# Optimization experiments

Measured on AMD Instinct MI355X. Metric: run time of the kernel, lower is better.

Reference implementation:

```python
import jax, jax.numpy as jnp
import numpy as np

B, T, N, DIN, HID, EMB, K, HOR, ODIM = 64, 12, 883, 1, 64, 10, 2, 12, 1


def setup_inputs() -> dict:
    key = jax.random.key(0)
    ks = jax.random.split(key, 12)
    s = 0.1  # keep gate pre-activations sane
    return dict(
        source=jax.random.normal(ks[0], (B, T, N, DIN), jnp.float32),
        node_emb=jax.random.normal(ks[1], (N, EMB), jnp.float32),
        w0_g=jax.random.normal(ks[2], (EMB, K, DIN + HID, 2 * HID), jnp.float32) * s,
        b0_g=jax.random.normal(ks[3], (EMB, 2 * HID), jnp.float32) * s,
        w0_c=jax.random.normal(ks[4], (EMB, K, DIN + HID, HID), jnp.float32) * s,
        b0_c=jax.random.normal(ks[5], (EMB, HID), jnp.float32) * s,
        w1_g=jax.random.normal(ks[6], (EMB, K, 2 * HID, 2 * HID), jnp.float32) * s,
        b1_g=jax.random.normal(ks[7], (EMB, 2 * HID), jnp.float32) * s,
        w1_c=jax.random.normal(ks[8], (EMB, K, 2 * HID, HID), jnp.float32) * s,
        b1_c=jax.random.normal(ks[9], (EMB, HID), jnp.float32) * s,
        conv_w=jax.random.normal(ks[10], (HOR * ODIM, 1, 1, HID), jnp.float32) * s,
        conv_b=jax.random.normal(ks[11], (HOR * ODIM,), jnp.float32) * s,
    )


def _supports(E):
    # adaptive adjacency: softmax(relu(E E^T)) row-wise, Chebyshev set [I, A, ...]
    A = jax.nn.softmax(jax.nn.relu(E @ E.T), axis=1)
    sup = [jnp.eye(E.shape[0], dtype=A.dtype), A]
    for _ in range(2, K):
        sup.append(2.0 * (A @ sup[-1]) - sup[-2])
    return jnp.stack(sup)  # [K, N, N]


def _gconv(x, E, sup, wpool, bpool):
    # x: [B,N,Cin] -> [B,N,Cout]; node-specific weights pooled from embeddings
    w = jnp.einsum('nd,dkio->nkio', E, wpool)          # [N,K,Cin,Cout]
    b = E @ bpool                                      # [N,Cout]
    xg = jnp.einsum('knm,bmc->bnkc', sup, x)           # [B,N,K,Cin]
    return jnp.einsum('bnki,nkio->bno', xg, w) + b


def _cell(x, h, E, sup, wg, bg, wc, bc):
    zr = jax.nn.sigmoid(_gconv(jnp.concatenate([x, h], -1), E, sup, wg, bg))
    z, r = jnp.split(zr, 2, axis=-1)
    hc = jnp.tanh(_gconv(jnp.concatenate([x, z * h], -1), E, sup, wc, bc))
    return r * h + (1.0 - r) * hc


def reference(source, node_emb, w0_g, b0_g, w0_c, b0_c, w1_g, b1_g, w1_c, b1_c, conv_w, conv_b):
    sup = _supports(node_emb)
    cur = jnp.transpose(source, (1, 0, 2, 3))  # [T,B,N,C]
    for wg, bg, wc, bc in ((w0_g, b0_g, w0_c, b0_c), (w1_g, b1_g, w1_c, b1_c)):
        h0 = jnp.zeros((source.shape[0], N, HID), source.dtype)

        def step(h, xt, wg=wg, bg=bg, wc=wc, bc=bc):
            hn = _cell(xt, h, node_emb, sup, wg, bg, wc, bc)
            return hn, hn

        _, cur = jax.lax.scan(step, h0, cur)  # [T,B,N,HID]
    last = cur[-1]  # [B,N,HID]
    # Conv2d(1, HOR*ODIM, kernel=(1,HID)) over [B,1,N,HID] == contraction over HID
    out = jnp.einsum('bnh,oh->bon', last, conv_w[:, 0, 0, :]) + conv_b[None, :, None]
    out = out.reshape(-1, HOR, ODIM, N).transpose(0, 1, 3, 2)  # [B,HOR,N,ODIM]
    return out
```

## Files before the change

kernel.cpp:

```cpp
#include <hip/hip_runtime.h>
#include <cstddef>

#define NN 883
#define BB 64
#define TT 12
#define EMB 10
#define KPAD 896

typedef short short8 __attribute__((ext_vector_type(8)));
typedef _Float16 half8 __attribute__((ext_vector_type(8)));
typedef float f32x4 __attribute__((ext_vector_type(4)));

__device__ __forceinline__ void split_f16(float v, _Float16* hp, _Float16* lp) {
  _Float16 h = (_Float16)v;
  *hp = h;
  *lp = (_Float16)(v - (float)h);
}

__global__ __launch_bounds__(256) void adj_kernel(const float* __restrict__ E,
                                                  _Float16* __restrict__ Ah,
                                                  _Float16* __restrict__ Al) {
  const int n = blockIdx.x;
  const int tid = threadIdx.x;
  __shared__ float sE[EMB];
  __shared__ float sred[256];
  if (tid < EMB) sE[tid] = E[n * EMB + tid];
  __syncthreads();
  float d[4];
  float lmax = 0.0f;
#pragma unroll
  for (int q = 0; q < 4; ++q) {
    int m = tid + q * 256;
    d[q] = 0.0f;
    if (m < NN) {
      float s = 0.0f;
#pragma unroll
      for (int e = 0; e < EMB; ++e) s += sE[e] * E[m * EMB + e];
      d[q] = fmaxf(s, 0.0f);
      lmax = fmaxf(lmax, d[q]);
    }
  }
  sred[tid] = lmax;
  __syncthreads();
  for (int s = 128; s > 0; s >>= 1) {
    if (tid < s) sred[tid] = fmaxf(sred[tid], sred[tid + s]);
    __syncthreads();
  }
  const float mx = sred[0];
  __syncthreads();
  float lsum = 0.0f;
#pragma unroll
  for (int q = 0; q < 4; ++q) {
    int m = tid + q * 256;
    if (m < NN) {
      d[q] = expf(d[q] - mx);
      lsum += d[q];
    }
  }
  sred[tid] = lsum;
  __syncthreads();
  for (int s = 128; s > 0; s >>= 1) {
    if (tid < s) sred[tid] += sred[tid + s];
    __syncthreads();
  }
  const float inv = 1.0f / sred[0];
#pragma unroll
  for (int q = 0; q < 4; ++q) {
    int m = tid + q * 256;
    if (m < KPAD) {
      float v = (m < NN) ? d[q] * inv : 0.0f;
      split_f16(v, &Ah[(size_t)n * KPAD + m], &Al[(size_t)n * KPAD + m]);
    }
  }
}

__global__ __launch_bounds__(256) void mfma_gemm3(const _Float16* __restrict__ Ah,
                                                  const _Float16* __restrict__ Al,
                                                  const _Float16* __restrict__ Xh,
                                                  const _Float16* __restrict__ Xl,
                                                  _Float16* __restrict__ Gh,
                                                  _Float16* __restrict__ Gl, int L) {
  __shared__ _Float16 sA[2][128][40];
  __shared__ _Float16 sX[2][4][128][8];
  const int tid = threadIdx.x;
  const int lane = tid & 63;
  const int wid = tid >> 6;
  const int wm = (wid >> 1) * 64, wn = (wid & 1) * 64;
  const int bm = blockIdx.y * 128;
  const int bl = blockIdx.x * 128;
  const int l15 = lane & 15, l4 = lane >> 4;

  f32x4 acc[4][4] = {};

  const int xlp = (tid & 63) * 2;
  const int xko = tid >> 6;

  for (int k0 = 0; k0 < KPAD; k0 += 32) {
    __syncthreads();
#pragma unroll
    for (int p = 0; p < 2; ++p) {
      int i = tid + p * 256;
      int m = i >> 2, k8 = (i & 3) * 8;
      *(half8*)&sA[0][m][k8] = *(const half8*)&Ah[(size_t)(bm + m) * KPAD + k0 + k8];
      *(half8*)&sA[1][m][k8] = *(const half8*)&Al[(size_t)(bm + m) * KPAD + k0 + k8];
    }
    {
      int gl = bl + xlp;
      int kb = k0 + xko * 8;
#pragma unroll
      for (int buf = 0; buf < 2; ++buf) {
        const _Float16* Xp = buf ? Xl : Xh;
        unsigned int v[8];
#pragma unroll
        for (int j = 0; j < 8; ++j)
          v[j] = *(const unsigned int*)&Xp[(size_t)(kb + j) * L + gl];
        short8 lo, hi;
#pragma unroll
        for (int j = 0; j < 8; ++j) {
          lo[j] = (short)(v[j] & 0xFFFFu);
          hi[j] = (short)(v[j] >> 16);
        }
        *(short8*)&sX[buf][xko][xlp][0] = lo;
        *(short8*)&sX[buf][xko][xlp + 1][0] = hi;
      }
    }
    __syncthreads();
    half8 afh[4], afl[4], bfh[4], bfl[4];
#pragma unroll
    for (int mi = 0; mi < 4; ++mi) {
      afh[mi] = *(half8*)&sA[0][wm + mi * 16 + l15][l4 * 8];
      afl[mi] = *(half8*)&sA[1][wm + mi * 16 + l15][l4 * 8];
    }
#pragma unroll
    for (int ni = 0; ni < 4; ++ni) {
      bfh[ni] = *(half8*)&sX[0][l4][wn + ni * 16 + l15][0];
      bfl[ni] = *(half8*)&sX[1][l4][wn + ni * 16 + l15][0];
    }
#pragma unroll
    for (int mi = 0; mi < 4; ++mi)
#pragma unroll
      for (int ni = 0; ni < 4; ++ni) {
        acc[mi][ni] = __builtin_amdgcn_mfma_f32_16x16x32_f16(afh[mi], bfh[ni],
                                                             acc[mi][ni], 0, 0, 0);
        acc[mi][ni] = __builtin_amdgcn_mfma_f32_16x16x32_f16(afh[mi], bfl[ni],
                                                             acc[mi][ni], 0, 0, 0);
        acc[mi][ni] = __builtin_amdgcn_mfma_f32_16x16x32_f16(afl[mi], bfh[ni],
                                                             acc[mi][ni], 0, 0, 0);
      }
  }
#pragma unroll
  for (int mi = 0; mi < 4; ++mi) {
    int row0 = bm + wm + mi * 16 + l4 * 4;
#pragma unroll
    for (int ni = 0; ni < 4; ++ni) {
      int col = bl + wn + ni * 16 + l15;
#pragma unroll
      for (int r = 0; r < 4; ++r) {
        int row = row0 + r;
        if (row < NN)
          split_f16(acc[mi][ni][r], &Gh[(size_t)row * L + col],
                    &Gl[(size_t)row * L + col]);
      }
    }
  }
}

__global__ __launch_bounds__(256) void srcall_kernel(const float* __restrict__ src,
                                                     _Float16* __restrict__ Xsh,
                                                     _Float16* __restrict__ Xsl) {
  int i = blockIdx.x * 256 + threadIdx.x;
  if (i >= NN * BB * TT) return;
  int t = i % TT;
  int nb = i / TT;
  int b = nb & 63, n = nb >> 6;
  float v = src[((size_t)b * TT + t) * NN + n];
  size_t idx = (size_t)n * (TT * 512) + (size_t)t * 512 + (size_t)b * 8;
  split_f16(v, &Xsh[idx], &Xsl[idx]);
}

template <int CS, int CIN, int XSPLIT, int OW, int COUT>
__global__ __launch_bounds__(256) void wgen_pre(const float* __restrict__ E,
                                                const float* __restrict__ wpool,
                                                _Float16* __restrict__ Wh,
                                                _Float16* __restrict__ Wl) {
  constexpr int C = COUT / OW;
  constexpr int KD = 2 * CS;
  constexpr int KOW = KD / 8;
  const int bid = blockIdx.x;
  const int n = bid / C;
  const int oc = bid % C;
  if (n >= NN) return;
  const int och = oc * OW;
  const int tid = threadIdx.x;
  __shared__ float sE[EMB];
  if (tid < EMB) sE[tid] = E[n * EMB + tid];
  __syncthreads();
  _Float16* bh = Wh + ((size_t)n * C + oc) * ((size_t)KOW * OW * 8);
  _Float16* bl = Wl + ((size_t)n * C + oc) * ((size_t)KOW * OW * 8);
  const int o = tid & (OW - 1);
  for (int ko = tid / OW; ko < KOW; ko += 256 / OW) {
    half8 hv, lv;
#pragma unroll
    for (int j = 0; j < 8; ++j) {
      const int k = ko * 8 + j;
      const int kk = (k >= CS) ? 1 : 0;
      const int kc = k - kk * CS;
      int ii;
      if (CS == CIN) ii = kc;
      else ii = (kc == 0) ? 0 : ((kc >= XSPLIT) ? kc - XSPLIT + 1 : -1);
      float w = 0.0f;
      if (ii >= 0) {
        const float* wp = wpool + ((size_t)kk * CIN + ii) * COUT + och + o;
#pragma unroll
        for (int d = 0; d < EMB; ++d)
          w += sE[d] * wp[(size_t)d * (2 * CIN * COUT)];
      }
      _Float16 hh = (_Float16)w;
      hv[j] = hh;
      lv[j] = (_Float16)(w - (float)hh);
    }
    *(half8*)&bh[((size_t)ko * OW + o) * 8] = hv;
    *(half8*)&bl[((size_t)ko * OW + o) * 8] = lv;
  }
}

template <int CS, int CIN, int XSPLIT, int OW, bool GATE>
__global__ __launch_bounds__(256) void gconv_fused(
    const _Float16* __restrict__ IXh, const _Float16* __restrict__ IXl, int sIX, int oIX,
    const _Float16* __restrict__ IZh, const _Float16* __restrict__ IZl, int sIZ, int oIZ,
    const _Float16* __restrict__ DXh, const _Float16* __restrict__ DXl, int sDX, int oDX,
    const _Float16* __restrict__ DZh, const _Float16* __restrict__ DZl, int sDZ, int oDZ,
    const float* __restrict__ E, const float* __restrict__ wpool,
    const float* __restrict__ bpool, const float* __restrict__ ZRin,
    float* __restrict__ hstate, float* __restrict__ ZRout,
    _Float16* __restrict__ XAh, _Float16* __restrict__ XAl, int csA, int cbA,
    const _Float16* __restrict__ PWh, const _Float16* __restrict__ PWl) {
  constexpr int COUT = GATE ? 128 : 64;
  constexpr int C = COUT / OW;
  constexpr int KD = 2 * CS;
  constexpr int KP = (KD + 31) & ~31;
  constexpr int KOW = KD / 8;
  constexpr int NT = OW / 32;
  const int bid = blockIdx.x;
  const int xcd = bid & 7;
  const int rest = bid >> 3;
  const int oc = rest % C;
  const int nq = rest / C;
  const int n = nq * 8 + xcd;
  if (n >= NN) return;
  const int och = oc * OW;
  const int tid = threadIdx.x;
  const int lane = tid & 63, wid = tid >> 6;
  const int wm = (wid & 1) * 32;
  const int wn = (wid >> 1) * (OW / 2);
  const int l15 = lane & 15, l4 = lane >> 4;

  __shared__ float sE[EMB];
  __shared__ float sB[OW];
  __shared__ _Float16 sWh[KOW * OW * 8];
  __shared__ _Float16 sWl[KOW * OW * 8];

  if (tid < EMB) sE[tid] = E[n * EMB + tid];
  __syncthreads();

  if (PWh != nullptr) {
    const size_t wbase = ((size_t)n * C + oc) * ((size_t)KOW * OW * 8);
    for (int i = tid; i < KOW * OW; i += 256) {
      *(half8*)&sWh[(size_t)i * 8] = *(const half8*)&PWh[wbase + (size_t)i * 8];
      *(half8*)&sWl[(size_t)i * 8] = *(const half8*)&PWl[wbase + (size_t)i * 8];
    }
  } else {
    const int o = tid & (OW - 1);
    for (int ko = tid / OW; ko < KOW; ko += 256 / OW) {
      half8 hv, lv;
#pragma unroll
      for (int j = 0; j < 8; ++j) {
        const int k = ko * 8 + j;
        const int kk = (k >= CS) ? 1 : 0;
        const int kc = k - kk * CS;
        int ii;
        if (CS == CIN) ii = kc;
        else ii = (kc == 0) ? 0 : ((kc >= XSPLIT) ? kc - XSPLIT + 1 : -1);
        float w = 0.0f;
        if (ii >= 0) {
          const float* wp = wpool + ((size_t)kk * CIN + ii) * COUT + och + o;
#pragma unroll
          for (int d = 0; d < EMB; ++d)
            w += sE[d] * wp[(size_t)d * (2 * CIN * COUT)];
        }
        _Float16 hh = (_Float16)w;
        hv[j] = hh;
        lv[j] = (_Float16)(w - (float)hh);
      }
      *(half8*)&sWh[((size_t)ko * OW + o) * 8] = hv;
      *(half8*)&sWl[((size_t)ko * OW + o) * 8] = lv;
    }
  }
  if (tid < OW) {
    float bb = 0.0f;
#pragma unroll
    for (int d = 0; d < EMB; ++d) bb += sE[d] * bpool[d * COUT + och + tid];
    sB[tid] = bb;
  }
  __syncthreads();

  const size_t bIX = (size_t)n * sIX + (size_t)oIX * 512;
  const size_t bIZ = (size_t)n * sIZ + (size_t)oIZ * 512;
  const size_t bDX = (size_t)n * sDX + (size_t)oDX * 512;
  const size_t bDZ = (size_t)n * sDZ + (size_t)oDZ * 512;
  f32x4 acc[2][NT] = {};
  for (int k0 = 0; k0 < KP; k0 += 32) {
    const int kq = k0 + l4 * 8;
    half8 ah[2], al[2];
#pragma unroll
    for (int mt = 0; mt < 2; ++mt) {
      const int b = wm + mt * 16 + l15;
      if (kq < XSPLIT) {
        const size_t o = bIX + (size_t)(kq >> 3) * 512 + (size_t)b * 8;
        ah[mt] = *(const half8*)&IXh[o];
        al[mt] = *(const half8*)&IXl[o];
      } else if (kq < CS) {
        const size_t o = bIZ + (size_t)((kq - XSPLIT) >> 3) * 512 + (size_t)b * 8;
        ah[mt] = *(const half8*)&IZh[o];
        al[mt] = *(const half8*)&IZl[o];
      } else if (kq < CS + XSPLIT) {
        const size_t o = bDX + (size_t)((kq - CS) >> 3) * 512 + (size_t)b * 8;
        ah[mt] = *(const half8*)&DXh[o];
        al[mt] = *(const half8*)&DXl[o];
      } else if (kq < KD) {
        const size_t o =
            bDZ + (size_t)((kq - CS - XSPLIT) >> 3) * 512 + (size_t)b * 8;
        ah[mt] = *(const half8*)&DZh[o];
        al[mt] = *(const half8*)&DZl[o];
      } else {
        ah[mt] = (half8)(_Float16)0.f;
        al[mt] = (half8)(_Float16)0.f;
      }
    }
    const int koi = kq >> 3;
#pragma unroll
    for (int nt = 0; nt < NT; ++nt) {
      const int ol = wn + nt * 16 + l15;
      half8 bh, bl;
      if constexpr (KP == KD) {
        bh = *(const half8*)&sWh[((size_t)koi * OW + ol) * 8];
        bl = *(const half8*)&sWl[((size_t)koi * OW + ol) * 8];
      } else {
        if (kq < KD) {
          bh = *(const half8*)&sWh[((size_t)koi * OW + ol) * 8];
          bl = *(const half8*)&sWl[((size_t)koi * OW + ol) * 8];
        } else {
          bh = (half8)(_Float16)0.f;
          bl = (half8)(_Float16)0.f;
        }
      }
#pragma unroll
      for (int mt = 0; mt < 2; ++mt) {
        acc[mt][nt] =
            __builtin_amdgcn_mfma_f32_16x16x32_f16(ah[mt], bh, acc[mt][nt], 0, 0, 0);
        acc[mt][nt] =
            __builtin_amdgcn_mfma_f32_16x16x32_f16(ah[mt], bl, acc[mt][nt], 0, 0, 0);
        acc[mt][nt] =
            __builtin_amdgcn_mfma_f32_16x16x32_f16(al[mt], bh, acc[mt][nt], 0, 0, 0);
      }
    }
  }

#pragma unroll
  for (int mt = 0; mt < 2; ++mt) {
#pragma unroll
    for (int nt = 0; nt < NT; ++nt) {
      const int ol = wn + nt * 16 + l15;
      const int og = och + ol;
      const float bias = sB[ol];
#pragma unroll
      for (int r = 0; r < 4; ++r) {
        const int b = wm + mt * 16 + l4 * 4 + r;
        const size_t nb = (size_t)n * 64 + b;
        const float v = acc[mt][nt][r] + bias;
        if constexpr (GATE) {
          const float s = 1.0f / (1.0f + expf(-v));
          if (og < 64) {
            const float zh = s * hstate[nb * 64 + og];
            const int c2 = cbA + og;
            size_t ia = (size_t)n * 64 * csA + (size_t)(c2 >> 3) * 512 +
                        (size_t)b * 8 + (c2 & 7);
            split_f16(zh, &XAh[ia], &XAl[ia]);
          } else {
            ZRout[nb * 64 + (og - 64)] = s;
          }
        } else {
          const float hc = tanhf(v);
          const float rr = ZRin[nb * 64 + og];
          const float hold = hstate[nb * 64 + og];
          const float hn = rr * hold + (1.0f - rr) * hc;
          hstate[nb * 64 + og] = hn;
          const int cA = cbA + og;
          size_t ia = (size_t)n * 64 * csA + (size_t)(cA >> 3) * 512 +
                      (size_t)b * 8 + (cA & 7);
          split_f16(hn, &XAh[ia], &XAl[ia]);
        }
      }
    }
  }
}

__global__ __launch_bounds__(256) void head_kernel(const float* __restrict__ h1,
                                                   const float* __restrict__ cw,
                                                   const float* __restrict__ cb,
                                                   float* __restrict__ out) {
  int i = blockIdx.x * 256 + threadIdx.x;
  if (i >= BB * NN) return;
  int n = i % NN, b = i / NN;
  const float* hrow = h1 + ((size_t)n * 64 + b) * 64;
  float hv[64];
#pragma unroll
  for (int j = 0; j < 64; ++j) hv[j] = hrow[j];
  for (int o = 0; o < 12; ++o) {
    float s = cb[o];
#pragma unroll
    for (int j = 0; j < 64; ++j) s += hv[j] * cw[o * 64 + j];
    out[((size_t)b * 12 + o) * NN + n] = s;
  }
}

__global__ __launch_bounds__(256) void zero_f32(float* __restrict__ p, size_t count) {
  size_t i = (size_t)blockIdx.x * 256 + threadIdx.x;
  if (i < count) p[i] = 0.0f;
}
__global__ __launch_bounds__(256) void zero_u16(unsigned short* __restrict__ p,
                                                size_t count) {
  size_t i = (size_t)blockIdx.x * 256 + threadIdx.x;
  if (i < count) p[i] = 0;
}

extern "C" void kernel_launch(void* const* d_in, const int* in_sizes, int n_in,
                              void* d_out, int out_size, void* d_ws, size_t ws_size,
                              hipStream_t stream) {
  const float* src = (const float*)d_in[0];
  const float* E = (const float*)d_in[1];
  const float* w0g = (const float*)d_in[2];
  const float* b0g = (const float*)d_in[3];
  const float* w0c = (const float*)d_in[4];
  const float* b0c = (const float*)d_in[5];
  const float* w1g = (const float*)d_in[6];
  const float* b1g = (const float*)d_in[7];
  const float* w1c = (const float*)d_in[8];
  const float* b1c = (const float*)d_in[9];
  const float* cw = (const float*)d_in[10];
  const float* cb = (const float*)d_in[11];
  float* out = (float*)d_out;
  float* ws = (float*)d_ws;

  size_t off = 0;
  auto alloc = [&](size_t cnt) {
    float* p = ws + off;
    off += (cnt + 63) & ~(size_t)63;
    return p;
  };
  const int LS = TT * 512;
  const int L1 = 64 * 128;
  const int LZ = 64 * 64;
  _Float16* Ah = (_Float16*)alloc((size_t)KPAD * KPAD / 2);
  _Float16* Al = (_Float16*)alloc((size_t)KPAD * KPAD / 2);
  _Float16* Xsh = (_Float16*)alloc((size_t)KPAD * LS / 2);
  _Float16* Xsl = (_Float16*)alloc((size_t)KPAD * LS / 2);
  _Float16* Gxh = (_Float16*)alloc((size_t)KPAD * LS / 2);
  _Float16* Gxl = (_Float16*)alloc((size_t)KPAD * LS / 2);
  _Float16* X1ah = (_Float16*)alloc((size_t)KPAD * L1 / 2);
  _Float16* X1al = (_Float16*)alloc((size_t)KPAD * L1 / 2);
  _Float16* Xzh = (_Float16*)alloc((size_t)KPAD * LZ / 2);
  _Float16* Xzl = (_Float16*)alloc((size_t)KPAD * LZ / 2);
  _Float16* Gl1h = (_Float16*)alloc((size_t)KPAD * L1 / 2);
  _Float16* Gl1l = (_Float16*)alloc((size_t)KPAD * L1 / 2);
  _Float16* Gzh = (_Float16*)alloc((size_t)KPAD * LZ / 2);
  _Float16* Gzl = (_Float16*)alloc((size_t)KPAD * LZ / 2);
  float* ZR = alloc((size_t)NN * BB * 64);
  float* h0 = alloc((size_t)NN * BB * 64);
  float* h1 = alloc((size_t)NN * BB * 64);
  if (off * sizeof(float) > ws_size) return;

  const size_t wsfl = ws_size / sizeof(float);
  const size_t whalves[4] = {(size_t)NN * 18432, (size_t)NN * 9216,
                             (size_t)NN * 32768, (size_t)NN * 16384};
  const size_t avail = (wsfl > off) ? (wsfl - off) : 0;
  int best = 0;
  size_t bestsz = 0;
  for (int s = 1; s < 16; ++s) {
    size_t tot = 0;
    for (int f = 0; f < 4; ++f)
      if (s & (1 << f)) tot += whalves[f] + 128;
    if (tot <= avail && tot > bestsz) {
      bestsz = tot;
      best = s;
    }
  }
  _Float16 *W0gh = nullptr, *W0gl = nullptr, *W0ch = nullptr, *W0cl = nullptr;
  _Float16 *W1gh = nullptr, *W1gl = nullptr, *W1ch = nullptr, *W1cl = nullptr;
  if (best & 1) {
    W0gh = (_Float16*)alloc(whalves[0] / 2);
    W0gl = (_Float16*)alloc(whalves[0] / 2);
  }
  if (best & 2) {
    W0ch = (_Float16*)alloc(whalves[1] / 2);
    W0cl = (_Float16*)alloc(whalves[1] / 2);
  }
  if (best & 4) {
    W1gh = (_Float16*)alloc(whalves[2] / 2);
    W1gl = (_Float16*)alloc(whalves[2] / 2);
  }
  if (best & 8) {
    W1ch = (_Float16*)alloc(whalves[3] / 2);
    W1cl = (_Float16*)alloc(whalves[3] / 2);
  }

  adj_kernel<<<NN, 256, 0, stream>>>(E, Ah, Al);
  {
    size_t cx = (size_t)2 * KPAD * (LS + LS + L1 + LZ + L1 + LZ);
    size_t chh = (size_t)2 * NN * BB * 64;
    zero_u16<<<(int)((cx + 255) / 256), 256, 0, stream>>>((unsigned short*)Xsh, cx);
    zero_f32<<<(int)((chh + 255) / 256), 256, 0, stream>>>(h0, chh);
  }
  srcall_kernel<<<(NN * BB * TT + 255) / 256, 256, 0, stream>>>(src, Xsh, Xsl);
  mfma_gemm3<<<dim3(LS / 128, 7), 256, 0, stream>>>(Ah, Al, Xsh, Xsl, Gxh, Gxl, LS);
  if (W0gh) wgen_pre<72, 65, 8, 32, 128><<<NN * 4, 256, 0, stream>>>(E, w0g, W0gh, W0gl);
  if (W0ch) wgen_pre<72, 65, 8, 32, 64><<<NN * 2, 256, 0, stream>>>(E, w0c, W0ch, W0cl);
  if (W1gh) wgen_pre<128, 128, 64, 32, 128><<<NN * 4, 256, 0, stream>>>(E, w1g, W1gh, W1gl);
  if (W1ch) wgen_pre<128, 128, 64, 32, 64><<<NN * 2, 256, 0, stream>>>(E, w1c, W1ch, W1cl);

  const int gx1 = L1 / 128;
  const int gxz = LZ / 128;
  const int NQ8 = ((NN + 7) / 8) * 8;
  const int g_gate = NQ8 * 4;
  const int g_cand = NQ8 * 2;
  for (int t = 0; t < TT; ++t) {
    gconv_fused<72, 65, 8, 32, true><<<g_gate, 256, 0, stream>>>(
        Xsh, Xsl, LS, t, X1ah, X1al, L1, 0, Gxh, Gxl, LS, t, Gl1h, Gl1l, L1, 0,
        E, w0g, b0g, nullptr, h0, ZR, Xzh, Xzl, 64, 0, W0gh, W0gl);
    mfma_gemm3<<<dim3(gxz, 7), 256, 0, stream>>>(Ah, Al, Xzh, Xzl, Gzh, Gzl, LZ);
    gconv_fused<72, 65, 8, 32, false><<<g_cand, 256, 0, stream>>>(
        Xsh, Xsl, LS, t, Xzh, Xzl, LZ, 0, Gxh, Gxl, LS, t, Gzh, Gzl, LZ, 0,
        E, w0c, b0c, ZR, h0, nullptr, X1ah, X1al, 128, 0, W0ch, W0cl);
    mfma_gemm3<<<dim3(gx1, 7), 256, 0, stream>>>(Ah, Al, X1ah, X1al, Gl1h, Gl1l, L1);
    gconv_fused<128, 128, 64, 32, true><<<g_gate, 256, 0, stream>>>(
        X1ah, X1al, L1, 0, X1ah, X1al, L1, 8, Gl1h, Gl1l, L1, 0, Gl1h, Gl1l, L1, 8,
        E, w1g, b1g, nullptr, h1, ZR, Xzh, Xzl, 64, 0, W1gh, W1gl);
    mfma_gemm3<<<dim3(gxz, 7), 256, 0, stream>>>(Ah, Al, Xzh, Xzl, Gzh, Gzl, LZ);
    gconv_fused<128, 128, 64, 32, false><<<g_cand, 256, 0, stream>>>(
        X1ah, X1al, L1, 0, Xzh, Xzl, LZ, 0, Gl1h, Gl1l, L1, 0, Gzh, Gzl, LZ, 0,
        E, w1c, b1c, ZR, h1, nullptr, X1ah, X1al, 128, 64, W1ch, W1cl);
  }
  head_kernel<<<(BB * NN + 255) / 256, 256, 0, stream>>>(h1, cw, cb, out);
}
```

Before: 3.837 ms.

## Process two nodes per gconv block and drop fp32 hidden state buffers

Each gconv_fused block now handles two nodes, with each pair of waves owning one node's full 32-column output slice, so the per-node weight-generation setup is shared across twice the work. Grid size is halved. The separate fp32 hidden-state arrays are removed, and the old h is reconstructed from the split-f16 X1a buffer (hi+lo) that already stores it. This removes the hstate reads and writes and the zeroing kernel. The trade-off is doubled shared memory per block, which may lower occupancy, and small rounding differences because h is now held in split-f16 rather than fp32.

```diff
diff --git a/kernel.cpp b/kernel.cpp
--- a/kernel.cpp
+++ b/kernel.cpp
@@ -232,7 +232,8 @@
     const _Float16* __restrict__ DZh, const _Float16* __restrict__ DZl, int sDZ, int oDZ,
     const float* __restrict__ E, const float* __restrict__ wpool,
     const float* __restrict__ bpool, const float* __restrict__ ZRin,
-    float* __restrict__ hstate, float* __restrict__ ZRout,
+    const _Float16* __restrict__ Hh, const _Float16* __restrict__ Hl, int hb,
+    float* __restrict__ ZRout,
     _Float16* __restrict__ XAh, _Float16* __restrict__ XAl, int csA, int cbA,
     const _Float16* __restrict__ PWh, const _Float16* __restrict__ PWl) {
   constexpr int COUT = GATE ? 128 : 64;
@@ -240,39 +241,54 @@
   constexpr int KD = 2 * CS;
   constexpr int KP = (KD + 31) & ~31;
   constexpr int KOW = KD / 8;
-  constexpr int NT = OW / 32;
   const int bid = blockIdx.x;
   const int xcd = bid & 7;
   const int rest = bid >> 3;
   const int oc = rest % C;
-  const int nq = rest / C;
-  const int n = nq * 8 + xcd;
-  if (n >= NN) return;
+  const int pq = rest / C;
+  const int p = pq * 8 + xcd;
+  const int nA = p * 2;
+  if (nA >= NN) return;
   const int och = oc * OW;
   const int tid = threadIdx.x;
   const int lane = tid & 63, wid = tid >> 6;
+  const int ns = wid >> 1;
   const int wm = (wid & 1) * 32;
-  const int wn = (wid >> 1) * (OW / 2);
   const int l15 = lane & 15, l4 = lane >> 4;
-
-  __shared__ float sE[EMB];
-  __shared__ float sB[OW];
-  __shared__ _Float16 sWh[KOW * OW * 8];
-  __shared__ _Float16 sWl[KOW * OW * 8];
-
-  if (tid < EMB) sE[tid] = E[n * EMB + tid];
+  const int myn = nA + ns;
+  const int anode = (myn < NN) ? myn : nA;
+
+  __shared__ float sE[2][EMB];
+  __shared__ float sB[2][OW];
+  __shared__ _Float16 sWh[2][KOW * OW * 8];
+  __shared__ _Float16 sWl[2][KOW * OW * 8];
+
+  if (tid < 2 * EMB) {
+    const int s = tid / EMB, d = tid - s * EMB;
+    const int node = nA + s;
+    sE[s][d] = (node < NN) ? E[node * EMB + d] : 0.0f;
+  }
   __syncthreads();
 
   if (PWh != nullptr) {
-    const size_t wbase = ((size_t)n * C + oc) * ((size_t)KOW * OW * 8);
-    for (int i = tid; i < KOW * OW; i += 256) {
-      *(half8*)&sWh[(size_t)i * 8] = *(const half8*)&PWh[wbase + (size_t)i * 8];
-      *(half8*)&sWl[(size_t)i * 8] = *(const half8*)&PWl[wbase + (size_t)i * 8];
+    for (int i = tid; i < 2 * KOW * OW; i += 256) {
+      const int s = i / (KOW * OW);
+      const int r = i - s * (KOW * OW);
+      const int node = nA + s;
+      half8 hv = (half8)(_Float16)0.f, lv = (half8)(_Float16)0.f;
+      if (node < NN) {
+        const size_t wb =
+            ((size_t)node * C + oc) * ((size_t)KOW * OW * 8) + (size_t)r * 8;
+        hv = *(const half8*)&PWh[wb];
+        lv = *(const half8*)&PWl[wb];
+      }
+      *(half8*)&sWh[s][(size_t)r * 8] = hv;
+      *(half8*)&sWl[s][(size_t)r * 8] = lv;
     }
   } else {
     const int o = tid & (OW - 1);
     for (int ko = tid / OW; ko < KOW; ko += 256 / OW) {
-      half8 hv, lv;
+      half8 hv0, lv0, hv1, lv1;
 #pragma unroll
       for (int j = 0; j < 8; ++j) {
         const int k = ko * 8 + j;
@@ -281,34 +297,43 @@
         int ii;
         if (CS == CIN) ii = kc;
         else ii = (kc == 0) ? 0 : ((kc >= XSPLIT) ? kc - XSPLIT + 1 : -1);
-        float w = 0.0f;
+        float w0 = 0.0f, w1 = 0.0f;
         if (ii >= 0) {
           const float* wp = wpool + ((size_t)kk * CIN + ii) * COUT + och + o;
 #pragma unroll
-          for (int d = 0; d < EMB; ++d)
-            w += sE[d] * wp[(size_t)d * (2 * CIN * COUT)];
+          for (int d = 0; d < EMB; ++d) {
+            const float wv = wp[(size_t)d * (2 * CIN * COUT)];
+            w0 += sE[0][d] * wv;
+            w1 += sE[1][d] * wv;
+          }
         }
-        _Float16 hh = (_Float16)w;
-        hv[j] = hh;
-        lv[j] = (_Float16)(w - (float)hh);
-      }
-      *(half8*)&sWh[((size_t)ko * OW + o) * 8] = hv;
-      *(half8*)&sWl[((size_t)ko * OW + o) * 8] = lv;
-    }
-  }
-  if (tid < OW) {
+        _Float16 h0 = (_Float16)w0;
+        hv0[j] = h0;
+        lv0[j] = (_Float16)(w0 - (float)h0);
+        _Float16 h1 = (_Float16)w1;
+        hv1[j] = h1;
+        lv1[j] = (_Float16)(w1 - (float)h1);
+      }
+      *(half8*)&sWh[0][((size_t)ko * OW + o) * 8] = hv0;
+      *(half8*)&sWl[0][((size_t)ko * OW + o) * 8] = lv0;
+      *(half8*)&sWh[1][((size_t)ko * OW + o) * 8] = hv1;
+      *(half8*)&sWl[1][((size_t)ko * OW + o) * 8] = lv1;
+    }
+  }
+  if (tid < 2 * OW) {
+    const int s = tid / OW, o = tid - s * OW;
     float bb = 0.0f;
 #pragma unroll
-    for (int d = 0; d < EMB; ++d) bb += sE[d] * bpool[d * COUT + och + tid];
-    sB[tid] = bb;
-  }
-  __syncthreads();
-
-  const size_t bIX = (size_t)n * sIX + (size_t)oIX * 512;
-  const size_t bIZ = (size_t)n * sIZ + (size_t)oIZ * 512;
-  const size_t bDX = (size_t)n * sDX + (size_t)oDX * 512;
-  const size_t bDZ = (size_t)n * sDZ + (size_t)oDZ * 512;
-  f32x4 acc[2][NT] = {};
+    for (int d = 0; d < EMB; ++d) bb += sE[s][d] * bpool[d * COUT + och + o];
+    sB[s][o] = bb;
+  }
+  __syncthreads();
+
+  const size_t bIX = (size_t)anode * sIX + (size_t)oIX * 512;
+  const size_t bIZ = (size_t)anode * sIZ + (size_t)oIZ * 512;
+  const size_t bDX = (size_t)anode * sDX + (size_t)oDX * 512;
+  const size_t bDZ = (size_t)anode * sDZ + (size_t)oDZ * 512;
+  f32x4 acc[2][2] = {};
   for (int k0 = 0; k0 < KP; k0 += 32) {
     const int kq = k0 + l4 * 8;
     half8 ah[2], al[2];
@@ -338,84 +363,91 @@
       }
     }
     const int koi = kq >> 3;
-#pragma unroll
-    for (int nt = 0; nt < NT; ++nt) {
-      const int ol = wn + nt * 16 + l15;
-      half8 bh, bl;
-      if constexpr (KP == KD) {
-        bh = *(const half8*)&sWh[((size_t)koi * OW + ol) * 8];
-        bl = *(const half8*)&sWl[((size_t)koi * OW + ol) * 8];
+    half8 bh[2], bl[2];
+#pragma unroll
+    for (int nt = 0; nt < 2; ++nt) {
+      const int ol = nt * 16 + l15;
+      if (KP == KD || kq < KD) {
+        bh[nt] = *(const half8*)&sWh[ns][((size_t)koi * OW + ol) * 8];
+        bl[nt] = *(const half8*)&sWl[ns][((size_t)koi * OW + ol) * 8];
       } else {
-        if (kq < KD) {
-          bh = *(const half8*)&sWh[((size_t)koi * OW + ol) * 8];
-          bl = *(const half8*)&sWl[((size_t)koi * OW + ol) * 8];
-        } else {
-          bh = (half8)(_Float16)0.f;
-          bl = (half8)(_Float16)0.f;
+        bh[nt] = (half8)(_Float16)0.f;
+        bl[nt] = (half8)(_Float16)0.f;
+      }
+    }
+#pragma unroll
+    for (int mt = 0; mt < 2; ++mt)
+#pragma unroll
+      for (int nt = 0; nt < 2; ++nt) {
+        acc[mt][nt] =
+            __builtin_amdgcn_mfma_f32_16x16x32_f16(ah[mt], bh[nt], acc[mt][nt], 0, 0, 0);
+        acc[mt][nt] =
+            __builtin_amdgcn_mfma_f32_16x16x32_f16(ah[mt], bl[nt], acc[mt][nt], 0, 0, 0);
+        acc[mt][nt] =
+            __builtin_amdgcn_mfma_f32_16x16x32_f16(al[mt], bh[nt], acc[mt][nt], 0, 0, 0);
+      }
+  }
+
+  if (myn < NN) {
+#pragma unroll
+    for (int mt = 0; mt < 2; ++mt) {
+#pragma unroll
+      for (int nt = 0; nt < 2; ++nt) {
+        const int ol = nt * 16 + l15;
+        const int og = och + ol;
+        const float bias = sB[ns][ol];
+#pragma unroll
+        for (int r = 0; r < 4; ++r) {
+          const int b = wm + mt * 16 + l4 * 4 + r;
+          const size_t nb = (size_t)myn * 64 + b;
+          const float v = acc[mt][nt][r] + bias;
+          if constexpr (GATE) {
+            const float s = 1.0f / (1.0f + expf(-v));
+            if (og < 64) {
+              const int ch = hb + og;
+              const size_t ih = (size_t)myn * 8192 + (size_t)(ch >> 3) * 512 +
+                                (size_t)b * 8 + (ch & 7);
+              const float hold = (float)Hh[ih] + (float)Hl[ih];
+              const float zh = s * hold;
+              const int c2 = cbA + og;
+              size_t ia = (size_t)myn * 64 * csA + (size_t)(c2 >> 3) * 512 +
+                          (size_t)b * 8 + (c2 & 7);
+              split_f16(zh, &XAh[ia], &XAl[ia]);
+            } else {
+              ZRout[nb * 64 + (og - 64)] = s;
+            }
+          } else {
+            const float hc = tanhf(v);
+            const float rr = ZRin[nb * 64 + og];
+            const int cA = cbA + og;
+            const size_t ia = (size_t)myn * 64 * csA + (size_t)(cA >> 3) * 512 +
+                              (size_t)b * 8 + (cA & 7);
+            const float hold = (float)XAh[ia] + (float)XAl[ia];
+            const float hn = rr * hold + (1.0f - rr) * hc;
+            split_f16(hn, &XAh[ia], &XAl[ia]);
+          }
         }
       }
-#pragma unroll
-      for (int mt = 0; mt < 2; ++mt) {
-        acc[mt][nt] =
-            __builtin_amdgcn_mfma_f32_16x16x32_f16(ah[mt], bh, acc[mt][nt], 0, 0, 0);
-        acc[mt][nt] =
-            __builtin_amdgcn_mfma_f32_16x16x32_f16(ah[mt], bl, acc[mt][nt], 0, 0, 0);
-        acc[mt][nt] =
-            __builtin_amdgcn_mfma_f32_16x16x32_f16(al[mt], bh, acc[mt][nt], 0, 0, 0);
-      }
-    }
-  }
-
-#pragma unroll
-  for (int mt = 0; mt < 2; ++mt) {
-#pragma unroll
-    for (int nt = 0; nt < NT; ++nt) {
-      const int ol = wn + nt * 16 + l15;
-      const int og = och + ol;
-      const float bias = sB[ol];
-#pragma unroll
-      for (int r = 0; r < 4; ++r) {
-        const int b = wm + mt * 16 + l4 * 4 + r;
-        const size_t nb = (size_t)n * 64 + b;
-        const float v = acc[mt][nt][r] + bias;
-        if constexpr (GATE) {
-          const float s = 1.0f / (1.0f + expf(-v));
-          if (og < 64) {
-            const float zh = s * hstate[nb * 64 + og];
-            const int c2 = cbA + og;
-            size_t ia = (size_t)n * 64 * csA + (size_t)(c2 >> 3) * 512 +
-                        (size_t)b * 8 + (c2 & 7);
-            split_f16(zh, &XAh[ia], &XAl[ia]);
-          } else {
-            ZRout[nb * 64 + (og - 64)] = s;
-          }
-        } else {
-          const float hc = tanhf(v);
-          const float rr = ZRin[nb * 64 + og];
-          const float hold = hstate[nb * 64 + og];
-          const float hn = rr * hold + (1.0f - rr) * hc;
-          hstate[nb * 64 + og] = hn;
-          const int cA = cbA + og;
-          size_t ia = (size_t)n * 64 * csA + (size_t)(cA >> 3) * 512 +
-                      (size_t)b * 8 + (cA & 7);
-          split_f16(hn, &XAh[ia], &XAl[ia]);
-        }
-      }
-    }
-  }
-}
-
-__global__ __launch_bounds__(256) void head_kernel(const float* __restrict__ h1,
+    }
+  }
+}
+
+__global__ __launch_bounds__(256) void head_kernel(const _Float16* __restrict__ Hh,
+                                                   const _Float16* __restrict__ Hl,
                                                    const float* __restrict__ cw,
                                                    const float* __restrict__ cb,
                                                    float* __restrict__ out) {
   int i = blockIdx.x * 256 + threadIdx.x;
   if (i >= BB * NN) return;
   int n = i % NN, b = i / NN;
-  const float* hrow = h1 + ((size_t)n * 64 + b) * 64;
   float hv[64];
 #pragma unroll
-  for (int j = 0; j < 64; ++j) hv[j] = hrow[j];
+  for (int j = 0; j < 64; ++j) {
+    const int c = 64 + j;
+    const size_t ia =
+        (size_t)n * 8192 + (size_t)(c >> 3) * 512 + (size_t)b * 8 + (c & 7);
+    hv[j] = (float)Hh[ia] + (float)Hl[ia];
+  }
   for (int o = 0; o < 12; ++o) {
     float s = cb[o];
 #pragma unroll
@@ -424,10 +456,6 @@
   }
 }
 
-__global__ __launch_bounds__(256) void zero_f32(float* __restrict__ p, size_t count) {
-  size_t i = (size_t)blockIdx.x * 256 + threadIdx.x;
-  if (i < count) p[i] = 0.0f;
-}
 __global__ __launch_bounds__(256) void zero_u16(unsigned short* __restrict__ p,
                                                 size_t count) {
   size_t i = (size_t)blockIdx.x * 256 + threadIdx.x;
@@ -476,8 +504,6 @@
   _Float16* Gzh = (_Float16*)alloc((size_t)KPAD * LZ / 2);
   _Float16* Gzl = (_Float16*)alloc((size_t)KPAD * LZ / 2);
   float* ZR = alloc((size_t)NN * BB * 64);
-  float* h0 = alloc((size_t)NN * BB * 64);
-  float* h1 = alloc((size_t)NN * BB * 64);
   if (off * sizeof(float) > ws_size) return;
 
   const size_t wsfl = ws_size / sizeof(float);
@@ -517,9 +543,7 @@
   adj_kernel<<<NN, 256, 0, stream>>>(E, Ah, Al);
   {
     size_t cx = (size_t)2 * KPAD * (LS + LS + L1 + LZ + L1 + LZ);
-    size_t chh = (size_t)2 * NN * BB * 64;
     zero_u16<<<(int)((cx + 255) / 256), 256, 0, stream>>>((unsigned short*)Xsh, cx);
-    zero_f32<<<(int)((chh + 255) / 256), 256, 0, stream>>>(h0, chh);
   }
   srcall_kernel<<<(NN * BB * TT + 255) / 256, 256, 0, stream>>>(src, Xsh, Xsl);
   mfma_gemm3<<<dim3(LS / 128, 7), 256, 0, stream>>>(Ah, Al, Xsh, Xsl, Gxh, Gxl, LS);
@@ -530,25 +554,25 @@
 
   const int gx1 = L1 / 128;
   const int gxz = LZ / 128;
-  const int NQ8 = ((NN + 7) / 8) * 8;
-  const int g_gate = NQ8 * 4;
-  const int g_cand = NQ8 * 2;
+  const int PQ = (((NN + 1) / 2 + 7) / 8) * 8;
+  const int g_gate = PQ * 4;
+  const int g_cand = PQ * 2;
   for (int t = 0; t < TT; ++t) {
     gconv_fused<72, 65, 8, 32, true><<<g_gate, 256, 0, stream>>>(
         Xsh, Xsl, LS, t, X1ah, X1al, L1, 0, Gxh, Gxl, LS, t, Gl1h, Gl1l, L1, 0,
-        E, w0g, b0g, nullptr, h0, ZR, Xzh, Xzl, 64, 0, W0gh, W0gl);
+        E, w0g, b0g, nullptr, X1ah, X1al, 0, ZR, Xzh, Xzl, 64, 0, W0gh, W0gl);
     mfma_gemm3<<<dim3(gxz, 7), 256, 0, stream>>>(Ah, Al, Xzh, Xzl, Gzh, Gzl, LZ);
     gconv_fused<72, 65, 8, 32, false><<<g_cand, 256, 0, stream>>>(
         Xsh, Xsl, LS, t, Xzh, Xzl, LZ, 0, Gxh, Gxl, LS, t, Gzh, Gzl, LZ, 0,
-        E, w0c, b0c, ZR, h0, nullptr, X1ah, X1al, 128, 0, W0ch, W0cl);
+        E, w0c, b0c, ZR, nullptr, nullptr, 0, nullptr, X1ah, X1al, 128, 0, W0ch, W0cl);
     mfma_gemm3<<<dim3(gx1, 7), 256, 0, stream>>>(Ah, Al, X1ah, X1al, Gl1h, Gl1l, L1);
     gconv_fused<128, 128, 64, 32, true><<<g_gate, 256, 0, stream>>>(
         X1ah, X1al, L1, 0, X1ah, X1al, L1, 8, Gl1h, Gl1l, L1, 0, Gl1h, Gl1l, L1, 8,
-        E, w1g, b1g, nullptr, h1, ZR, Xzh, Xzl, 64, 0, W1gh, W1gl);
+        E, w1g, b1g, nullptr, X1ah, X1al, 64, ZR, Xzh, Xzl, 64, 0, W1gh, W1gl);
     mfma_gemm3<<<dim3(gxz, 7), 256, 0, stream>>>(Ah, Al, Xzh, Xzl, Gzh, Gzl, LZ);
     gconv_fused<128, 128, 64, 32, false><<<g_cand, 256, 0, stream>>>(
         X1ah, X1al, L1, 0, Xzh, Xzl, LZ, 0, Gl1h, Gl1l, L1, 0, Gzh, Gzl, LZ, 0,
-        E, w1c, b1c, ZR, h1, nullptr, X1ah, X1al, 128, 64, W1ch, W1cl);
-  }
-  head_kernel<<<(BB * NN + 255) / 256, 256, 0, stream>>>(h1, cw, cb, out);
-}
+        E, w1c, b1c, ZR, nullptr, nullptr, 0, nullptr, X1ah, X1al, 128, 64, W1ch, W1cl);
+  }
+  head_kernel<<<(BB * NN + 255) / 256, 256, 0, stream>>>(X1ah, X1al, cw, cb, out);
+}
```

New measurement: 3.782 ms. Within noise of the previous version (-1.4%).
